# Kernel tuning notes

Measured on AMD Instinct MI355X. Metric: run time of the kernel, lower is better.

Reference implementation:

```python
import jax, jax.numpy as jnp
import numpy as np

IN_FEATURES = 256
EMBED = 512
HEADS = 8
HEAD_DIM = EMBED // HEADS
BLOCKS = 2
FFN = 2048
CLASSES = 1000
NWIRES = 8
BATCH = 8
SEQ = 2048


def _posenc(seq, dim, dtype):
    pos = jnp.arange(seq, dtype=jnp.float32)[:, None]
    div = jnp.exp(jnp.arange(0, dim, 2, dtype=jnp.float32) * (-jnp.log(10000.0) / dim))
    pe = jnp.zeros((seq, dim), dtype=jnp.float32)
    pe = pe.at[:, 0::2].set(jnp.sin(pos * div))
    pe = pe.at[:, 1::2].set(jnp.cos(pos * div))
    return pe.astype(dtype)


def _layer_norm(x, g, b, eps=1e-5):
    mu = jnp.mean(x, axis=-1, keepdims=True)
    var = jnp.var(x, axis=-1, keepdims=True)
    return (x - mu) * jax.lax.rsqrt(var + eps) * g + b


def setup_inputs() -> dict:
    key = jax.random.key(0)
    ks = jax.random.split(key, 20)
    s = 0.02
    inp = {
        'x': jax.random.normal(ks[0], (BATCH, SEQ, IN_FEATURES), dtype=jnp.float32),
        'Wi': jax.random.normal(ks[1], (EMBED, IN_FEATURES), dtype=jnp.float32) * s,
        'bi': jnp.zeros((EMBED,), dtype=jnp.float32),
        'theta_a': jax.random.normal(ks[2], (BLOCKS, NWIRES), dtype=jnp.float32),
        'Wproj': jax.random.normal(ks[3], (BLOCKS, EMBED, NWIRES), dtype=jnp.float32) * s,
        'Wq': jax.random.normal(ks[4], (BLOCKS, EMBED, EMBED), dtype=jnp.float32) * s,
        'Wk': jax.random.normal(ks[5], (BLOCKS, EMBED, EMBED), dtype=jnp.float32) * s,
        'Wv': jax.random.normal(ks[6], (BLOCKS, EMBED, EMBED), dtype=jnp.float32) * s,
        'Wo': jax.random.normal(ks[7], (BLOCKS, EMBED, EMBED), dtype=jnp.float32) * s,
        'g1': jnp.ones((BLOCKS, EMBED), dtype=jnp.float32),
        'b1': jnp.zeros((BLOCKS, EMBED), dtype=jnp.float32),
        'phi': jax.random.normal(ks[8], (BLOCKS, NWIRES), dtype=jnp.float32),
        'W1': jax.random.normal(ks[9], (BLOCKS, FFN, NWIRES), dtype=jnp.float32) * s,
        'W2': jax.random.normal(ks[10], (BLOCKS, EMBED, FFN), dtype=jnp.float32) * s,
        'g2': jnp.ones((BLOCKS, EMBED), dtype=jnp.float32),
        'b2': jnp.zeros((BLOCKS, EMBED), dtype=jnp.float32),
        'Wc': jax.random.normal(ks[11], (CLASSES, EMBED), dtype=jnp.float32) * s,
        'bc': jnp.zeros((CLASSES,), dtype=jnp.float32),
    }
    return inp


def reference(x, Wi, bi, theta_a, Wproj, Wq, Wk, Wv, Wo, g1, b1, phi, W1, W2, g2, b2, Wc, bc):
    b, s, _ = x.shape
    h = jnp.einsum('bsf,ef->bse', x, Wi) + bi          # input_proj
    h = h + _posenc(s, EMBED, h.dtype)[None]           # positional encoding
    scale = 1.0 / np.sqrt(HEAD_DIM)
    for l in range(BLOCKS):
        # --- quantum attention sublayer ---
        # RX encode first NWIRES features + trainable RX per wire -> <Z> = cos(x + theta)
        q_out = jnp.cos(h[..., :NWIRES] + theta_a[l])  # [b,s,nw]
        x_q = jnp.einsum('bsw,ew->bse', q_out, Wproj[l])
        q = jnp.einsum('bse,fe->bsf', x_q, Wq[l]).reshape(b, s, HEADS, HEAD_DIM).transpose(0, 2, 1, 3)
        k = jnp.einsum('bse,fe->bsf', x_q, Wk[l]).reshape(b, s, HEADS, HEAD_DIM).transpose(0, 2, 1, 3)
        v = jnp.einsum('bse,fe->bsf', x_q, Wv[l]).reshape(b, s, HEADS, HEAD_DIM).transpose(0, 2, 1, 3)
        scores = jnp.einsum('bhqd,bhkd->bhqk', q, k) * scale
        attn = jax.nn.softmax(scores, axis=-1)
        out = jnp.einsum('bhqk,bhkd->bhqd', attn, v)
        out = out.transpose(0, 2, 1, 3).reshape(b, s, EMBED)
        attn_out = jnp.einsum('bse,fe->bsf', out, Wo[l])
        h = _layer_norm(h + attn_out, g1[l], b1[l])
        # --- quantum feed-forward sublayer ---
        # RY encode + trainable RY per wire -> <Z> = cos(x + phi)
        qf = jnp.cos(h[..., :NWIRES] + phi[l])         # [b,s,nw]
        f = jnp.einsum('bsw,fw->bsf', qf, W1[l])       # nw -> ffn
        f = jnp.einsum('bsf,ef->bse', jax.nn.relu(f), W2[l])
        h = _layer_norm(h + f, g2[l], b2[l])
    pooled = jnp.mean(h, axis=1)                        # [b, embed]
    logits = jnp.einsum('be,ce->bc', pooled, Wc) + bc
    return logits
```

## Files before the change

kernel.cpp:

```cpp
#include <hip/hip_runtime.h>
#include <hip/hip_bf16.h>
#include <math.h>

#define B_   8
#define S_   2048
#define T_   (B_*S_)
#define FIN  256
#define E_   512
#define H_   8
#define D_   64
#define FFN_ 2048
#define NC_  1000
#define NW_  8

typedef __attribute__((ext_vector_type(8))) short short8;
typedef __attribute__((ext_vector_type(4))) short short4v;
typedef __attribute__((ext_vector_type(4))) float f32x4;
typedef __attribute__((ext_vector_type(2))) unsigned int uint2v;
typedef __attribute__((ext_vector_type(4))) unsigned int uint4v;

__device__ __forceinline__ unsigned short f2bf(float f) {
    __hip_bfloat16 h = __float2bfloat16(f);
    return __builtin_bit_cast(unsigned short, h);
}
__device__ __forceinline__ float bf2f(unsigned short u) {
    return __builtin_bit_cast(float, (unsigned int)u << 16);
}

__device__ __forceinline__ unsigned cvtpk_bf16(float lo, float hi) {
    unsigned r;
    asm("v_cvt_pk_bf16_f32 %0, %1, %2" : "=v"(r) : "v"(lo), "v"(hi));
    return r;
}

#if defined(__has_builtin)
#if __has_builtin(__builtin_amdgcn_permlane32_swap) && __has_builtin(__builtin_amdgcn_permlane16_swap)
#define HAVE_PLSWAP 1
#endif
#endif

__device__ __forceinline__ void lswap32(unsigned &a, unsigned &b) {
#if defined(HAVE_PLSWAP)
    uint2v t = __builtin_amdgcn_permlane32_swap(a, b, false, false);
    a = t[0]; b = t[1];
#else
    unsigned as = (unsigned)__shfl_xor((int)a, 32);
    unsigned bs = (unsigned)__shfl_xor((int)b, 32);
    bool hi = (threadIdx.x & 32) != 0;
    unsigned na = hi ? bs : a;
    unsigned nb = hi ? b  : as;
    a = na; b = nb;
#endif
}
__device__ __forceinline__ void lswap16(unsigned &a, unsigned &b) {
#if defined(HAVE_PLSWAP)
    uint2v t = __builtin_amdgcn_permlane16_swap(a, b, false, false);
    a = t[0]; b = t[1];
#else
    unsigned as = (unsigned)__shfl_xor((int)a, 16);
    unsigned bs = (unsigned)__shfl_xor((int)b, 16);
    bool hi = (threadIdx.x & 16) != 0;
    unsigned na = hi ? bs : a;
    unsigned nb = hi ? b  : as;
    a = na; b = nb;
#endif
}

__device__ __forceinline__ void gld16(void* l, const void* g) {
    __builtin_amdgcn_global_load_lds(
        (const __attribute__((address_space(1))) unsigned int*)g,
        (__attribute__((address_space(3))) unsigned int*)l,
        16, 0, 0);
}

#if defined(__has_builtin)
#if __has_builtin(__builtin_amdgcn_mfma_f32_16x16x16bf16_1k)
#define HAVE_MFMA16 1
#endif
#endif

__device__ __forceinline__ f32x4 mfma16(short4v a, short4v b, f32x4 c) {
#ifdef HAVE_MFMA16
    return __builtin_amdgcn_mfma_f32_16x16x16bf16_1k(a, b, c, 0, 0, 0);
#else
    short8 a8 = {a[0], a[1], a[2], a[3], 0, 0, 0, 0};
    short8 b8 = {b[0], b[1], b[2], b[3], 0, 0, 0, 0};
    return __builtin_amdgcn_mfma_f32_16x16x32_bf16(a8, b8, c, 0, 0, 0);
#endif
}

__global__ __launch_bounds__(256)
void cvt_all(const float* __restrict__ x,  const float* __restrict__ Wi,
             const float* __restrict__ Wo, const float* __restrict__ W2,
             const float* __restrict__ W1,
             unsigned short* xb, unsigned short* Wib,
             unsigned short* Wob, unsigned short* W2b, unsigned short* W1b)
{
    int g = blockIdx.x*256 + threadIdx.x;
    const float* s; unsigned short* d; int o;
    if      (g < 1048576) { s = x;  d = xb;  o = g; }
    else if (g < 1081344) { s = Wi; d = Wib; o = g - 1048576; }
    else if (g < 1212416) { s = Wo; d = Wob; o = g - 1081344; }
    else if (g < 1736704) { s = W2; d = W2b; o = g - 1212416; }
    else                  { s = W1; d = W1b; o = g - 1736704; }
    float4 vv = ((const float4*)s)[o];
    ushort4 u;
    u.x = f2bf(vv.x); u.y = f2bf(vv.y); u.z = f2bf(vv.z); u.w = f2bf(vv.w);
    ((ushort4*)d)[o] = u;
}

__global__ __launch_bounds__(64)
void weff_kernel(const float* __restrict__ Wq, const float* __restrict__ Wk,
                 const float* __restrict__ Wv, const float* __restrict__ Wproj,
                 unsigned short* __restrict__ Weff)
{
    const int f = blockIdx.x, l = blockIdx.y, which = blockIdx.z;
    const int lane = threadIdx.x;
    const float* W = (which == 0 ? Wq : which == 1 ? Wk : Wv)
                     + (size_t)l*E_*E_ + (size_t)f*E_;
    const float* P = Wproj + (size_t)l*E_*NW_;
    const int wv = lane & 7;
    float s = 0.f;
    for (int e = (lane >> 3)*64; e < (lane >> 3)*64 + 64; e++)
        s += W[e] * P[e*NW_ + wv];
    #pragma unroll
    for (int off = 8; off < 64; off <<= 1) s += __shfl_xor(s, off);
    const float scale = (which == 0) ? 0.18033688011112042f : 1.f;
    if (lane < 8)
        Weff[((size_t)(which*2 + l)*E_ + f)*NW_ + lane] = f2bf(s * scale);
}

__global__ __launch_bounds__(64)
void gram_kernel(const unsigned short* __restrict__ Weff, unsigned short* __restrict__ G)
{
    const int hh = blockIdx.x, l = blockIdx.y;
    const int lane = threadIdx.x;
    const int w = lane >> 3, wp = lane & 7;
    const unsigned short* Wq_e = Weff + (size_t)(0*2 + l)*E_*NW_ + (size_t)hh*64*NW_;
    const unsigned short* Wk_e = Weff + (size_t)(1*2 + l)*E_*NW_ + (size_t)hh*64*NW_;
    float s = 0.f;
    for (int d = 0; d < 64; d++)
        s += bf2f(Wq_e[d*NW_ + w]) * bf2f(Wk_e[d*NW_ + wp]);
    G[(size_t)(l*8 + hh)*64 + w*8 + wp] = f2bf(s);
}

__global__ __launch_bounds__(64)
void wov_kernel(const float* __restrict__ Wo, const unsigned short* __restrict__ Weff,
                unsigned short* __restrict__ WoV)
{
    const int f = blockIdx.x, l = blockIdx.y;
    const int lane = threadIdx.x;
    const int hh = lane >> 3, w = lane & 7;
    const float* wrow = Wo + (size_t)l*E_*E_ + (size_t)f*E_ + hh*64;
    const unsigned short* Wv_e = Weff + (size_t)(2*2 + l)*E_*NW_ + (size_t)hh*64*NW_;
    float s = 0.f;
    for (int d = 0; d < 64; d++)
        s += wrow[d] * bf2f(Wv_e[d*NW_ + w]);
    WoV[(size_t)(l*E_ + f)*64 + lane] = f2bf(s);
}

__global__ __launch_bounds__(256)
void qc_small(const unsigned short* __restrict__ h, const float* __restrict__ theta,
              const unsigned short* __restrict__ G,
              unsigned short* __restrict__ c8, unsigned short* __restrict__ c8T,
              unsigned short* __restrict__ gkb)
{
    const int tid = threadIdx.x;
    const int t0 = blockIdx.x * 32;
    __shared__ float cs[32][8];
    __shared__ float Gs[512];
    {
        int tl = tid >> 3, wv2 = tid & 7;
        cs[tl][wv2] = cosf(bf2f(h[(size_t)(t0 + tl)*E_ + wv2]) + theta[wv2]);
        Gs[tid]       = bf2f(G[tid]);
        Gs[tid + 256] = bf2f(G[tid + 256]);
    }
    __syncthreads();
    const int tl = tid >> 3, hh = tid & 7;
    const int bb = (t0 + tl) >> 11, ss = (t0 + tl) & (S_ - 1);
    float c[8];
    #pragma unroll
    for (int i = 0; i < 8; i++) c[i] = cs[tl][i];
    unsigned short u[8] __attribute__((aligned(16)));
    #pragma unroll
    for (int w = 0; w < 8; w++) {
        float s = 0.f;
        #pragma unroll
        for (int wp = 0; wp < 8; wp++) s += Gs[hh*64 + w*8 + wp] * c[wp];
        u[w] = f2bf(s);
    }
    *(float4*)&gkb[((size_t)(bb*H_ + hh)*S_ + ss)*8] = *(float4*)u;
    if (tid < 32) {
        unsigned short v[8] __attribute__((aligned(16)));
        #pragma unroll
        for (int i = 0; i < 8; i++) v[i] = f2bf(cs[tid][i]);
        *(float4*)&c8[(size_t)(t0 + tid)*8] = *(float4*)v;
    } else if (tid < 40) {
        int w = tid - 32;
        unsigned short v[32] __attribute__((aligned(16)));
        #pragma unroll
        for (int s = 0; s < 32; s++) v[s] = f2bf(cs[s][w]);
        unsigned short* dst = c8T + ((size_t)(t0 >> 11)*8 + w)*S_ + (t0 & (S_ - 1));
        #pragma unroll
        for (int cq = 0; cq < 4; cq++) *(float4*)(dst + cq*8) = *(float4*)&v[cq*8];
    }
}

template<int TC_BF16, int MODE>
__global__ __launch_bounds__(256)
void gemm_mfma(const unsigned short* __restrict__ A,
               const unsigned short* __restrict__ Bm,
               void* __restrict__ Cv, int M, int N, int K,
               float scale, const float* __restrict__ bias)
{
    __shared__ char Lraw[32768];
    unsigned short* Al = (unsigned short*)Lraw;
    unsigned short* Bl = (unsigned short*)(Lraw + 16384);
    float* Ot = (float*)Lraw;

    const int tid  = threadIdx.x;
    const int lane = tid & 63;
    const int w    = tid >> 6;
    const int wx   = w & 1, wy = w >> 1;
    int bx, by;
    {
        int nx = gridDim.x;
        int bid = blockIdx.y * nx + blockIdx.x;
        int rpx = gridDim.y >> 3;
        int xcd = bid & 7, idx = bid >> 3;
        by = xcd * rpx + idx / nx;
        bx = idx % nx;
    }
    const int rowBase = by * 128;
    const int colBase = bx * 128;
    const int l15  = lane & 15;
    const int quad = lane >> 4;
    const int srow = lane >> 2;
    const int gch  = (lane & 3) ^ ((srow >> 1) & 3);
    const int swz  = (l15 >> 1) & 3;

    f32x4 acc[4][4] = {};

    #pragma unroll
    for (int it = 0; it < 2; it++) {
        int rb = it*64 + w*16;
        gld16(&Al[rb*32], A  + (size_t)(rowBase + rb + srow)*K + gch*8);
        gld16(&Bl[rb*32], Bm + (size_t)(colBase + rb + srow)*K + gch*8);
    }

    for (int k0 = 0; k0 < K; k0 += 32) {
        const int cur = (k0 >> 5) & 1;
        __syncthreads();
        if (k0 + 32 < K) {
            #pragma unroll
            for (int it = 0; it < 2; it++) {
                int rb = it*64 + w*16;
                gld16(&Al[(1-cur)*4096 + rb*32], A  + (size_t)(rowBase + rb + srow)*K + k0 + 32 + gch*8);
                gld16(&Bl[(1-cur)*4096 + rb*32], Bm + (size_t)(colBase + rb + srow)*K + k0 + 32 + gch*8);
            }
        }
        short8 af[4], bfr[4];
        #pragma unroll
        for (int mi = 0; mi < 4; mi++)
            af[mi] = *(const short8*)&Al[cur*4096 + (wy*64 + mi*16 + l15)*32 + ((quad ^ swz) << 3)];
        #pragma unroll
        for (int ni = 0; ni < 4; ni++)
            bfr[ni] = *(const short8*)&Bl[cur*4096 + (wx*64 + ni*16 + l15)*32 + ((quad ^ swz) << 3)];
        #pragma unroll
        for (int mi = 0; mi < 4; mi++)
            #pragma unroll
            for (int ni = 0; ni < 4; ni++)
                acc[mi][ni] = __builtin_amdgcn_mfma_f32_16x16x32_bf16(
                    af[mi], bfr[ni], acc[mi][ni], 0, 0, 0);
    }

    #pragma unroll
    for (int mi = 0; mi < 4; mi++) {
        __syncthreads();
        #pragma unroll
        for (int ni = 0; ni < 4; ni++) {
            #pragma unroll
            for (int r = 0; r < 4; r++) {
                float v = acc[mi][ni][r] * scale;
                if (MODE == 1) {
                    int row = rowBase + wy*64 + mi*16 + quad*4 + r;
                    int col = colBase + wx*64 + ni*16 + l15;
                    int s = row & (S_ - 1);
                    float freq = __expf(-0.017988946039244957f * (float)(col & ~1));
                    float ang = (float)s * freq;
                    v += bias[col] + ((col & 1) ? cosf(ang) : sinf(ang));
                }
                Ot[(wy*16 + quad*4 + r)*132 + wx*64 + ni*16 + l15] = v;
            }
        }
        __syncthreads();
        {
            int rl = tid >> 3, c0 = (tid & 7) * 16;
            int grow = rowBase + (rl >> 4)*64 + mi*16 + (rl & 15);
            float vv[16];
            #pragma unroll
            for (int j = 0; j < 4; j++)
                *(float4*)&vv[j*4] = *(const float4*)&Ot[rl*132 + c0 + j*4];
            if (TC_BF16) {
                unsigned short u[16] __attribute__((aligned(16)));
                #pragma unroll
                for (int i = 0; i < 16; i++) u[i] = f2bf(vv[i]);
                unsigned short* dst = (unsigned short*)Cv + (size_t)grow*N + colBase + c0;
                *(float4*)dst       = *(float4*)&u[0];
                *(float4*)(dst + 8) = *(float4*)&u[8];
            } else {
                float* dst = (float*)Cv + (size_t)grow*N + colBase + c0;
                #pragma unroll
                for (int j = 0; j < 4; j++)
                    *(float4*)(dst + j*4) = *(const float4*)&vv[j*4];
            }
        }
    }
}

__global__ __launch_bounds__(256)
void wo_ln(const unsigned short* __restrict__ yout,
           const unsigned short* __restrict__ WoV,
           unsigned short* __restrict__ h,
           const float* __restrict__ g, const float* __restrict__ b)
{
    __shared__ float Ot[16*520];
    const int tid  = threadIdx.x;
    const int lane = tid & 63;
    const int w    = tid >> 6;
    const int l15  = lane & 15;
    const int quad = lane >> 4;
    const size_t t0 = (size_t)blockIdx.x * 32;

    short8 af[2][2];
    #pragma unroll
    for (int mi = 0; mi < 2; mi++)
        #pragma unroll
        for (int kb = 0; kb < 2; kb++)
            af[mi][kb] = *(const short8*)&yout[(t0 + mi*16 + l15)*64 + kb*32 + quad*8];

    f32x4 acc[2][8] = {};
    #pragma unroll
    for (int ni = 0; ni < 8; ni++)
        #pragma unroll
        for (int kb = 0; kb < 2; kb++) {
            short8 bf8 = *(const short8*)&WoV[(size_t)(w*128 + ni*16 + l15)*64 + kb*32 + quad*8];
            acc[0][ni] = __builtin_amdgcn_mfma_f32_16x16x32_bf16(af[0][kb], bf8, acc[0][ni], 0, 0, 0);
            acc[1][ni] = __builtin_amdgcn_mfma_f32_16x16x32_bf16(af[1][kb], bf8, acc[1][ni], 0, 0, 0);
        }

    #pragma unroll
    for (int p = 0; p < 2; p++) {
        __syncthreads();
        #pragma unroll
        for (int ni = 0; ni < 8; ni++)
            #pragma unroll
            for (int r = 0; r < 4; r++)
                Ot[(quad*4 + r)*520 + w*128 + ni*16 + l15] = acc[p][ni][r];
        __syncthreads();
        const int tk = tid >> 4, u = tid & 15;
        const size_t trow = t0 + p*16 + tk;
        float x[32];
        float s = 0.f, sq = 0.f;
        #pragma unroll
        for (int j = 0; j < 8; j++) {
            int c = u*4 + j*64;
            ushort4 hv = *(const ushort4*)&h[trow*E_ + c];
            float4 at = *(const float4*)&Ot[tk*520 + c];
            float v0 = bf2f(hv.x) + at.x;
            float v1 = bf2f(hv.y) + at.y;
            float v2 = bf2f(hv.z) + at.z;
            float v3 = bf2f(hv.w) + at.w;
            x[j*4+0] = v0; x[j*4+1] = v1; x[j*4+2] = v2; x[j*4+3] = v3;
            s  += v0 + v1 + v2 + v3;
            sq += v0*v0 + v1*v1 + v2*v2 + v3*v3;
        }
        #pragma unroll
        for (int off = 1; off < 16; off <<= 1) {
            s  += __shfl_xor(s,  off);
            sq += __shfl_xor(sq, off);
        }
        float mu   = s * (1.f/E_);
        float var  = sq * (1.f/E_) - mu*mu;
        float rstd = rsqrtf(var + 1e-5f);
        #pragma unroll
        for (int j = 0; j < 8; j++) {
            int c = u*4 + j*64;
            float4 gv = *(const float4*)&g[c];
            float4 bv = *(const float4*)&b[c];
            ushort4 ov;
            ov.x = f2bf((x[j*4+0] - mu)*rstd*gv.x + bv.x);
            ov.y = f2bf((x[j*4+1] - mu)*rstd*gv.y + bv.y);
            ov.z = f2bf((x[j*4+2] - mu)*rstd*gv.z + bv.z);
            ov.w = f2bf((x[j*4+3] - mu)*rstd*gv.w + bv.w);
            *(ushort4*)&h[trow*E_ + c] = ov;
        }
    }
}

__global__ __launch_bounds__(256)
void gemm_w2f(const unsigned short* __restrict__ h, const float* __restrict__ phi,
              const unsigned short* __restrict__ W1b,
              const unsigned short* __restrict__ W2b,
              unsigned short* __restrict__ tmp)
{
    __shared__ char Lraw[17408];
    unsigned short* Wl = (unsigned short*)Lraw;
    float* Ot = (float*)Lraw;

    const int tid  = threadIdx.x;
    const int lane = tid & 63;
    const int w    = tid >> 6;
    const int tx   = w & 1, ty = w >> 1;
    const int l15  = lane & 15;
    const int quad = lane >> 4;
    const int srow = lane >> 2;
    const int gch  = (lane & 3) ^ ((srow >> 1) & 3);
    const int swz  = (l15 >> 1) & 3;

    const int bid = blockIdx.x;
    const int xcd = bid & 7;
    const int eb  = xcd >> 1;
    const int tb  = (xcd & 1) * 128 + (bid >> 3);
    const int tBase = tb * 64;
    const int eBase = eb * 128;

    short4v cosfr[2];
    #pragma unroll
    for (int nt = 0; nt < 2; nt++) {
        short4v c = {0,0,0,0};
        if (quad < 2) {
            int tok = tBase + ty*32 + nt*16 + l15;
            #pragma unroll
            for (int i = 0; i < 4; i++) {
                int wv = quad*4 + i;
                c[i] = (short)f2bf(cosf(bf2f(h[(size_t)tok*E_ + wv]) + phi[wv]));
            }
        }
        cosfr[nt] = c;
    }

    #pragma unroll
    for (int it = 0; it < 2; it++) {
        int rb = w*32 + it*16;
        gld16(&Wl[rb*32], W2b + (size_t)(eBase + rb + srow)*FFN_ + gch*8);
    }

    const f32x4 fzero = {0.f, 0.f, 0.f, 0.f};
    short4v w1fA[2] = {{0,0,0,0},{0,0,0,0}};

    auto ffn1_pack = [&](short8* pfr_out) {
        unsigned Pm[2][4];
        #pragma unroll
        for (int nt = 0; nt < 2; nt++) {
            #pragma unroll
            for (int jb = 0; jb < 2; jb++) {
                f32x4 c = mfma16(w1fA[jb], cosfr[nt], fzero);
                Pm[nt][jb*2]   = cvtpk_bf16(fmaxf(c[0], 0.f), fmaxf(c[1], 0.f));
                Pm[nt][jb*2+1] = cvtpk_bf16(fmaxf(c[2], 0.f), fmaxf(c[3], 0.f));
            }
            lswap32(Pm[nt][0], Pm[nt][2]); lswap32(Pm[nt][1], Pm[nt][3]);
            lswap16(Pm[nt][0], Pm[nt][2]); lswap16(Pm[nt][1], Pm[nt][3]);
            uint4v u = { Pm[nt][0], Pm[nt][1], Pm[nt][2], Pm[nt][3] };
            pfr_out[nt] = __builtin_bit_cast(short8, u);
        }
    };
    auto load_w1f = [&](int k0) {
        #pragma unroll
        for (int jb = 0; jb < 2; jb++)
            if (quad < 2)
                w1fA[jb] = *(const short4v*)&W1b[(size_t)(k0 + jb*16 + l15)*NW_ + quad*4];
    };

    load_w1f(0);
    short8 pf_cur[2], pf_next[2];
    ffn1_pack(pf_cur);
    load_w1f(32);

    f32x4 acc[4][2] = {};

    for (int k0 = 0; k0 < FFN_; k0 += 32) {
        const int cur = (k0 >> 5) & 1;
        __syncthreads();
        if (k0 + 32 < FFN_) {
            #pragma unroll
            for (int it = 0; it < 2; it++) {
                int rb = w*32 + it*16;
                gld16(&Wl[(1-cur)*4096 + rb*32],
                      W2b + (size_t)(eBase + rb + srow)*FFN_ + k0 + 32 + gch*8);
            }
            ffn1_pack(pf_next);
            if (k0 + 64 < FFN_) load_w1f(k0 + 64);
        }
        #pragma unroll
        for (int et = 0; et < 4; et++) {
            short8 wf = *(const short8*)&Wl[cur*4096 + (tx*64 + et*16 + l15)*32
                                             + ((quad ^ swz) << 3)];
            #pragma unroll
            for (int nt = 0; nt < 2; nt++)
                acc[et][nt] = __builtin_amdgcn_mfma_f32_16x16x32_bf16(
                    wf, pf_cur[nt], acc[et][nt], 0, 0, 0);
        }
        #pragma unroll
        for (int nt = 0; nt < 2; nt++) pf_cur[nt] = pf_next[nt];
    }

    #pragma unroll
    for (int et = 0; et < 4; et++) {
        __syncthreads();
        #pragma unroll
        for (int nt = 0; nt < 2; nt++)
            #pragma unroll
            for (int r = 0; r < 4; r++)
                Ot[(ty*32 + nt*16 + l15)*33 + tx*16 + quad*4 + r] = acc[et][nt][r];
        __syncthreads();
        int token = tid >> 2, q4 = tid & 3;
        unsigned short u[8] __attribute__((aligned(16)));
        #pragma unroll
        for (int i = 0; i < 8; i++) u[i] = f2bf(Ot[token*33 + q4*8 + i]);
        unsigned short* dst = tmp + (size_t)(tBase + token)*E_ + eBase
                              + (q4 >> 1)*64 + et*16 + (q4 & 1)*8;
        *(float4*)dst = *(float4*)&u[0];
    }
}

__global__ __launch_bounds__(256)
void flash_q(const unsigned short* __restrict__ c8,
             const unsigned short* __restrict__ c8T,
             const unsigned short* __restrict__ gkb,
             unsigned short* __restrict__ yout)
{
    const int tid  = threadIdx.x;
    const int lane = tid & 63;
    const int wv   = tid >> 6;
    const int l15  = lane & 15;
    const int quad = lane >> 4;
    const int bid  = blockIdx.x;
    const int xcd  = bid & 7;
    const int rest = bid >> 3;
    const int combo = xcd * 8 + (rest >> 4);
    const int qt = rest & 15;
    const int hh = combo & 7;
    const int bb = combo >> 3;
    const size_t qrow0 = (size_t)bb*S_ + (size_t)qt*128;
    const unsigned short* gkp  = gkb + (size_t)(bb*H_ + hh)*S_*NW_;
    const unsigned short* c8Tp = c8T + (size_t)bb*8*S_;

    short4v cqfr[2] = {{0,0,0,0},{0,0,0,0}};
    if (quad < 2) {
        #pragma unroll
        for (int mi = 0; mi < 2; mi++)
            cqfr[mi] = *(const short4v*)&c8[(qrow0 + wv*32 + mi*16 + l15)*NW_ + quad*4];
    }
    const short8 ones8 = {(short)0x3F80, (short)0x3F80, (short)0x3F80, (short)0x3F80,
                          (short)0x3F80, (short)0x3F80, (short)0x3F80, (short)0x3F80};
    f32x4 y[2] = {};

    for (int kt = 0; kt < S_/64; kt++) {
        f32x4 Sc[2][4] = {};
        #pragma unroll
        for (int nt = 0; nt < 4; nt++) {
            short4v gkf = {0,0,0,0};
            if (quad < 2)
                gkf = *(const short4v*)&gkp[(size_t)(kt*64 + nt*16 + l15)*NW_ + quad*4];
            Sc[0][nt] = mfma16(gkf, cqfr[0], Sc[0][nt]);
            Sc[1][nt] = mfma16(gkf, cqfr[1], Sc[1][nt]);
        }
        unsigned Pm[2][8];
        #pragma unroll
        for (int mi = 0; mi < 2; mi++)
            #pragma unroll
            for (int nt = 0; nt < 4; nt++) {
                float e0 = __builtin_amdgcn_exp2f(Sc[mi][nt][0]);
                float e1 = __builtin_amdgcn_exp2f(Sc[mi][nt][1]);
                float e2 = __builtin_amdgcn_exp2f(Sc[mi][nt][2]);
                float e3 = __builtin_amdgcn_exp2f(Sc[mi][nt][3]);
                Pm[mi][nt*2]   = cvtpk_bf16(e0, e1);
                Pm[mi][nt*2+1] = cvtpk_bf16(e2, e3);
            }
        #pragma unroll
        for (int mi = 0; mi < 2; mi++) {
            lswap32(Pm[mi][0], Pm[mi][2]); lswap32(Pm[mi][1], Pm[mi][3]);
            lswap32(Pm[mi][4], Pm[mi][6]); lswap32(Pm[mi][5], Pm[mi][7]);
            lswap16(Pm[mi][0], Pm[mi][2]); lswap16(Pm[mi][1], Pm[mi][3]);
            lswap16(Pm[mi][4], Pm[mi][6]); lswap16(Pm[mi][5], Pm[mi][7]);
        }
        short8 pf[2][2];
        #pragma unroll
        for (int mi = 0; mi < 2; mi++)
            #pragma unroll
            for (int kb = 0; kb < 2; kb++) {
                uint4v u = { Pm[mi][kb*4], Pm[mi][kb*4+1], Pm[mi][kb*4+2], Pm[mi][kb*4+3] };
                pf[mi][kb] = __builtin_bit_cast(short8, u);
            }
        #pragma unroll
        for (int kb = 0; kb < 2; kb++) {
            short8 a8 = {0,0,0,0,0,0,0,0};
            if (l15 < 8)
                a8 = *(const short8*)&c8Tp[(size_t)l15*S_ + kt*64 + kb*32 + quad*8];
            else if (l15 == 8)
                a8 = ones8;
            y[0] = __builtin_amdgcn_mfma_f32_16x16x32_bf16(a8, pf[0][kb], y[0], 0, 0, 0);
            y[1] = __builtin_amdgcn_mfma_f32_16x16x32_bf16(a8, pf[1][kb], y[1], 0, 0, 0);
        }
    }

    #pragma unroll
    for (int mi = 0; mi < 2; mi++) {
        float rs = __shfl(y[mi][0], 32 + l15);
        float inv = 1.f / rs;
        if (quad < 2) {
            unsigned d0 = cvtpk_bf16(y[mi][0]*inv, y[mi][1]*inv);
            unsigned d1 = cvtpk_bf16(y[mi][2]*inv, y[mi][3]*inv);
            unsigned* dst = (unsigned*)&yout[(qrow0 + wv*32 + mi*16 + l15)*64 + hh*8 + quad*4];
            dst[0] = d0; dst[1] = d1;
        }
    }
}

__global__ __launch_bounds__(256)
void add_ln(unsigned short* __restrict__ h, const unsigned short* __restrict__ delta,
            const float* __restrict__ g, const float* __restrict__ b)
{
    const int lane = threadIdx.x & 63;
    const int t = blockIdx.x*4 + (threadIdx.x >> 6);
    const size_t base = (size_t)t*E_ + lane*8;
    uint4 hv = *(const uint4*)&h[base];
    uint4 dv = *(const uint4*)&delta[base];
    float x[8];
    #pragma unroll
    for (int i = 0; i < 4; i++) {
        unsigned hu = ((const unsigned*)&hv)[i], du = ((const unsigned*)&dv)[i];
        x[2*i]   = bf2f((unsigned short)(hu & 0xffff)) + bf2f((unsigned short)(du & 0xffff));
        x[2*i+1] = bf2f((unsigned short)(hu >> 16))    + bf2f((unsigned short)(du >> 16));
    }
    float s = 0.f, sq = 0.f;
    #pragma unroll
    for (int i = 0; i < 8; i++) { s += x[i]; sq += x[i]*x[i]; }
    #pragma unroll
    for (int off = 1; off < 64; off <<= 1) {
        s  += __shfl_xor(s,  off);
        sq += __shfl_xor(sq, off);
    }
    float mu  = s * (1.f/E_);
    float var = sq * (1.f/E_) - mu*mu;
    float rstd = rsqrtf(var + 1e-5f);
    float4 g0 = *(const float4*)&g[lane*8], g1 = *(const float4*)&g[lane*8 + 4];
    float4 b0 = *(const float4*)&b[lane*8], b1 = *(const float4*)&b[lane*8 + 4];
    float gg[8] = {g0.x,g0.y,g0.z,g0.w,g1.x,g1.y,g1.z,g1.w};
    float bb[8] = {b0.x,b0.y,b0.z,b0.w,b1.x,b1.y,b1.z,b1.w};
    uint4 ov;
    #pragma unroll
    for (int i = 0; i < 4; i++) {
        unsigned lo = f2bf((x[2*i]   - mu)*rstd*gg[2*i]   + bb[2*i]);
        unsigned hi = f2bf((x[2*i+1] - mu)*rstd*gg[2*i+1] + bb[2*i+1]);
        ((unsigned*)&ov)[i] = lo | (hi << 16);
    }
    *(uint4*)&h[base] = ov;
}

__global__ __launch_bounds__(256)
void pool_partial(const unsigned short* __restrict__ h, float* __restrict__ part)
{
    const int chunk = blockIdx.x, bb = blockIdx.y, tid = threadIdx.x;
    for (int e = tid; e < E_; e += 256) {
        const unsigned short* p = h + ((size_t)bb*S_ + (size_t)chunk*128)*E_ + e;
        float s = 0.f;
        for (int r = 0; r < 128; r++) s += bf2f(p[(size_t)r*E_]);
        part[(size_t)(bb*16 + chunk)*E_ + e] = s;
    }
}

__global__ __launch_bounds__(256)
void pool_final(const float* __restrict__ part, float* __restrict__ pooled)
{
    const int bb = blockIdx.x, tid = threadIdx.x;
    for (int e = tid; e < E_; e += 256) {
        float s = 0.f;
        #pragma unroll
        for (int c = 0; c < 16; c++) s += part[(size_t)(bb*16 + c)*E_ + e];
        pooled[bb*E_ + e] = s * (1.f/S_);
    }
}

__global__ __launch_bounds__(64)
void classify(const float* __restrict__ pooled, const float* __restrict__ Wc,
              const float* __restrict__ bc, float* __restrict__ out)
{
    const int c = blockIdx.x, bb = blockIdx.y, lane = threadIdx.x;
    const float* p = pooled + bb*E_;
    const float* wc = Wc + (size_t)c*E_;
    float s = 0.f;
    for (int e = lane; e < E_; e += 64) s += p[e]*wc[e];
    #pragma unroll
    for (int off = 1; off < 64; off <<= 1) s += __shfl_xor(s, off);
    if (lane == 0) out[bb*NC_ + c] = s + bc[c];
}

extern "C" void kernel_launch(void* const* d_in, const int* in_sizes, int n_in,
                              void* d_out, int out_size, void* d_ws, size_t ws_size,
                              hipStream_t stream)
{
    const float* x       = (const float*)d_in[0];
    const float* Wi      = (const float*)d_in[1];
    const float* bi      = (const float*)d_in[2];
    const float* theta_a = (const float*)d_in[3];
    const float* Wproj   = (const float*)d_in[4];
    const float* Wq      = (const float*)d_in[5];
    const float* Wk      = (const float*)d_in[6];
    const float* Wv      = (const float*)d_in[7];
    const float* Wo      = (const float*)d_in[8];
    const float* g1      = (const float*)d_in[9];
    const float* b1      = (const float*)d_in[10];
    const float* phi     = (const float*)d_in[11];
    const float* W1      = (const float*)d_in[12];
    const float* W2      = (const float*)d_in[13];
    const float* g2      = (const float*)d_in[14];
    const float* b2      = (const float*)d_in[15];
    const float* Wc      = (const float*)d_in[16];
    const float* bc      = (const float*)d_in[17];
    float* out = (float*)d_out;

    char* ws = (char*)d_ws;
    const size_t MB = 1024u*1024u;
    unsigned short* h      = (unsigned short*)(ws + 0*MB);
    unsigned short* tmp    = (unsigned short*)(ws + 16*MB);
    unsigned short* c8     = (unsigned short*)(ws + 32*MB);
    unsigned short* c8T    = (unsigned short*)(ws + 33*MB);
    unsigned short* gkb    = (unsigned short*)(ws + 34*MB);
    unsigned short* yout   = (unsigned short*)(ws + 48*MB);
    unsigned short* xb     = (unsigned short*)(ws + 96*MB);
    unsigned short* Wib    = (unsigned short*)(ws + 104*MB);
    unsigned short* Wob    = (unsigned short*)(ws + 105*MB);
    unsigned short* W2b    = (unsigned short*)(ws + 106*MB);
    unsigned short* W1b    = (unsigned short*)(ws + 110*MB);
    unsigned short* Weff   = (unsigned short*)(ws + 111*MB);
    unsigned short* Gbuf   = (unsigned short*)(ws + 111*MB + 64*1024);
    unsigned short* WoV    = (unsigned short*)(ws + 111*MB + 128*1024);
    float*          part   = (float*)(ws + 112*MB);
    float*          pooled = (float*)(ws + 112*MB + 512*1024);

    cvt_all<<<6816, 256, 0, stream>>>(x, Wi, Wo, W2, W1, xb, Wib, Wob, W2b, W1b);
    weff_kernel<<<dim3(E_, 2, 3), 64, 0, stream>>>(Wq, Wk, Wv, Wproj, Weff);
    gram_kernel<<<dim3(H_, 2), 64, 0, stream>>>(Weff, Gbuf);
    wov_kernel<<<dim3(E_, 2), 64, 0, stream>>>(Wo, Weff, WoV);

    gemm_mfma<1,1><<<dim3(E_/128, T_/128), 256, 0, stream>>>(
        xb, Wib, h, T_, E_, FIN, 1.f, bi);

    for (int l = 0; l < 2; l++) {
        qc_small<<<T_/32, 256, 0, stream>>>(h, theta_a + l*NW_, Gbuf + (size_t)l*512,
                                            c8, c8T, gkb);
        flash_q<<<(S_/128)*H_*B_, 256, 0, stream>>>(c8, c8T, gkb, yout);
        wo_ln<<<T_/32, 256, 0, stream>>>(yout, WoV + (size_t)l*E_*64, h,
                                         g1 + l*E_, b1 + l*E_);

        gemm_w2f<<<1024, 256, 0, stream>>>(h, phi + l*NW_,
                                           W1b + (size_t)l*FFN_*NW_,
                                           W2b + (size_t)l*E_*FFN_, tmp);
        add_ln<<<T_/4, 256, 0, stream>>>(h, tmp, g2 + l*E_, b2 + l*E_);
    }

    pool_partial<<<dim3(16, B_), 256, 0, stream>>>(h, part);
    pool_final<<<B_, 256, 0, stream>>>(part, pooled);
    classify<<<dim3(NC_, B_), 64, 0, stream>>>(pooled, Wc, bc, out);
}
```

Before: 560.6 us.

## Fuse FFN W2 GEMM with residual add and LayerNorm per full-row token tile

The W2 GEMM kernel now computes all 512 output columns for a 32-token tile, so the residual add and LayerNorm can run in its epilogue, which lets the separate add_ln kernel and the tmp round trip through global memory be removed. The FFN1 activations are recomputed each k-step instead of being software-pipelined, and the unused Wo bf16 conversion is dropped from cvt_all. In exchange, each block now streams the whole W2 matrix, LDS use grows to about 65KB, and the tiles are smaller (32 tokens), which may lower occupancy and add W2 traffic. The kernel reads h and writes h in place, which is safe only because each block reads its cos inputs and residual from its own rows.

```diff
diff --git a/kernel.cpp b/kernel.cpp
--- a/kernel.cpp
+++ b/kernel.cpp
@@ -91,18 +91,16 @@
 
 __global__ __launch_bounds__(256)
 void cvt_all(const float* __restrict__ x,  const float* __restrict__ Wi,
-             const float* __restrict__ Wo, const float* __restrict__ W2,
-             const float* __restrict__ W1,
+             const float* __restrict__ W2, const float* __restrict__ W1,
              unsigned short* xb, unsigned short* Wib,
-             unsigned short* Wob, unsigned short* W2b, unsigned short* W1b)
+             unsigned short* W2b, unsigned short* W1b)
 {
     int g = blockIdx.x*256 + threadIdx.x;
     const float* s; unsigned short* d; int o;
     if      (g < 1048576) { s = x;  d = xb;  o = g; }
     else if (g < 1081344) { s = Wi; d = Wib; o = g - 1048576; }
-    else if (g < 1212416) { s = Wo; d = Wob; o = g - 1081344; }
-    else if (g < 1736704) { s = W2; d = W2b; o = g - 1212416; }
-    else                  { s = W1; d = W1b; o = g - 1736704; }
+    else if (g < 1605632) { s = W2; d = W2b; o = g - 1081344; }
+    else                  { s = W1; d = W1b; o = g - 1605632; }
     float4 vv = ((const float4*)s)[o];
     ushort4 u;
     u.x = f2bf(vv.x); u.y = f2bf(vv.y); u.z = f2bf(vv.z); u.w = f2bf(vv.w);
@@ -399,19 +397,19 @@
 }
 
 __global__ __launch_bounds__(256)
-void gemm_w2f(const unsigned short* __restrict__ h, const float* __restrict__ phi,
-              const unsigned short* __restrict__ W1b,
-              const unsigned short* __restrict__ W2b,
-              unsigned short* __restrict__ tmp)
-{
-    __shared__ char Lraw[17408];
+void w2f_ln(const unsigned short* __restrict__ hin, const float* __restrict__ phi,
+            const unsigned short* __restrict__ W1b,
+            const unsigned short* __restrict__ W2b,
+            unsigned short* __restrict__ h,
+            const float* __restrict__ g, const float* __restrict__ b)
+{
+    __shared__ char Lraw[66816];
     unsigned short* Wl = (unsigned short*)Lraw;
     float* Ot = (float*)Lraw;
 
     const int tid  = threadIdx.x;
     const int lane = tid & 63;
     const int w    = tid >> 6;
-    const int tx   = w & 1, ty = w >> 1;
     const int l15  = lane & 15;
     const int quad = lane >> 4;
     const int srow = lane >> 2;
@@ -419,108 +417,141 @@
     const int swz  = (l15 >> 1) & 3;
 
     const int bid = blockIdx.x;
-    const int xcd = bid & 7;
-    const int eb  = xcd >> 1;
-    const int tb  = (xcd & 1) * 128 + (bid >> 3);
-    const int tBase = tb * 64;
-    const int eBase = eb * 128;
+    const int tBase = ((bid & 7)*64 + (bid >> 3)) * 32;
 
     short4v cosfr[2];
     #pragma unroll
     for (int nt = 0; nt < 2; nt++) {
         short4v c = {0,0,0,0};
         if (quad < 2) {
-            int tok = tBase + ty*32 + nt*16 + l15;
+            int tok = tBase + nt*16 + l15;
             #pragma unroll
             for (int i = 0; i < 4; i++) {
                 int wv = quad*4 + i;
-                c[i] = (short)f2bf(cosf(bf2f(h[(size_t)tok*E_ + wv]) + phi[wv]));
+                c[i] = (short)f2bf(cosf(bf2f(hin[(size_t)tok*E_ + wv]) + phi[wv]));
             }
         }
         cosfr[nt] = c;
     }
 
     #pragma unroll
-    for (int it = 0; it < 2; it++) {
-        int rb = w*32 + it*16;
-        gld16(&Wl[rb*32], W2b + (size_t)(eBase + rb + srow)*FFN_ + gch*8);
-    }
+    for (int it = 0; it < 8; it++) {
+        int rb = w*128 + it*16;
+        gld16(&Wl[rb*32], W2b + (size_t)(rb + srow)*FFN_ + gch*8);
+    }
+    short4v w1f[2] = {{0,0,0,0},{0,0,0,0}};
+    #pragma unroll
+    for (int jb = 0; jb < 2; jb++)
+        if (quad < 2)
+            w1f[jb] = *(const short4v*)&W1b[(size_t)(jb*16 + l15)*NW_ + quad*4];
 
     const f32x4 fzero = {0.f, 0.f, 0.f, 0.f};
-    short4v w1fA[2] = {{0,0,0,0},{0,0,0,0}};
-
-    auto ffn1_pack = [&](short8* pfr_out) {
-        unsigned Pm[2][4];
-        #pragma unroll
-        for (int nt = 0; nt < 2; nt++) {
-            #pragma unroll
-            for (int jb = 0; jb < 2; jb++) {
-                f32x4 c = mfma16(w1fA[jb], cosfr[nt], fzero);
-                Pm[nt][jb*2]   = cvtpk_bf16(fmaxf(c[0], 0.f), fmaxf(c[1], 0.f));
-                Pm[nt][jb*2+1] = cvtpk_bf16(fmaxf(c[2], 0.f), fmaxf(c[3], 0.f));
-            }
-            lswap32(Pm[nt][0], Pm[nt][2]); lswap32(Pm[nt][1], Pm[nt][3]);
-            lswap16(Pm[nt][0], Pm[nt][2]); lswap16(Pm[nt][1], Pm[nt][3]);
-            uint4v u = { Pm[nt][0], Pm[nt][1], Pm[nt][2], Pm[nt][3] };
-            pfr_out[nt] = __builtin_bit_cast(short8, u);
-        }
-    };
-    auto load_w1f = [&](int k0) {
-        #pragma unroll
-        for (int jb = 0; jb < 2; jb++)
-            if (quad < 2)
-                w1fA[jb] = *(const short4v*)&W1b[(size_t)(k0 + jb*16 + l15)*NW_ + quad*4];
-    };
-
-    load_w1f(0);
-    short8 pf_cur[2], pf_next[2];
-    ffn1_pack(pf_cur);
-    load_w1f(32);
-
-    f32x4 acc[4][2] = {};
+    f32x4 acc[8][2] = {};
 
     for (int k0 = 0; k0 < FFN_; k0 += 32) {
         const int cur = (k0 >> 5) & 1;
         __syncthreads();
         if (k0 + 32 < FFN_) {
             #pragma unroll
-            for (int it = 0; it < 2; it++) {
-                int rb = w*32 + it*16;
-                gld16(&Wl[(1-cur)*4096 + rb*32],
-                      W2b + (size_t)(eBase + rb + srow)*FFN_ + k0 + 32 + gch*8);
-            }
-            ffn1_pack(pf_next);
-            if (k0 + 64 < FFN_) load_w1f(k0 + 64);
-        }
-        #pragma unroll
-        for (int et = 0; et < 4; et++) {
-            short8 wf = *(const short8*)&Wl[cur*4096 + (tx*64 + et*16 + l15)*32
+            for (int it = 0; it < 8; it++) {
+                int rb = w*128 + it*16;
+                gld16(&Wl[(1-cur)*16384 + rb*32],
+                      W2b + (size_t)(rb + srow)*FFN_ + k0 + 32 + gch*8);
+            }
+        }
+        short8 pfr[2];
+        #pragma unroll
+        for (int nt = 0; nt < 2; nt++) {
+            unsigned Pm[4];
+            #pragma unroll
+            for (int jb = 0; jb < 2; jb++) {
+                f32x4 c = mfma16(w1f[jb], cosfr[nt], fzero);
+                Pm[jb*2]   = cvtpk_bf16(fmaxf(c[0], 0.f), fmaxf(c[1], 0.f));
+                Pm[jb*2+1] = cvtpk_bf16(fmaxf(c[2], 0.f), fmaxf(c[3], 0.f));
+            }
+            lswap32(Pm[0], Pm[2]); lswap32(Pm[1], Pm[3]);
+            lswap16(Pm[0], Pm[2]); lswap16(Pm[1], Pm[3]);
+            uint4v u = { Pm[0], Pm[1], Pm[2], Pm[3] };
+            pfr[nt] = __builtin_bit_cast(short8, u);
+        }
+        if (k0 + 32 < FFN_) {
+            #pragma unroll
+            for (int jb = 0; jb < 2; jb++)
+                if (quad < 2)
+                    w1f[jb] = *(const short4v*)&W1b[(size_t)(k0 + 32 + jb*16 + l15)*NW_ + quad*4];
+        }
+        #pragma unroll
+        for (int et = 0; et < 8; et++) {
+            short8 wf = *(const short8*)&Wl[cur*16384 + (w*128 + et*16 + l15)*32
                                              + ((quad ^ swz) << 3)];
             #pragma unroll
             for (int nt = 0; nt < 2; nt++)
                 acc[et][nt] = __builtin_amdgcn_mfma_f32_16x16x32_bf16(
-                    wf, pf_cur[nt], acc[et][nt], 0, 0, 0);
-        }
-        #pragma unroll
-        for (int nt = 0; nt < 2; nt++) pf_cur[nt] = pf_next[nt];
-    }
-
-    #pragma unroll
-    for (int et = 0; et < 4; et++) {
-        __syncthreads();
+                    wf, pfr[nt], acc[et][nt], 0, 0, 0);
+        }
+    }
+
+    __syncthreads();
+    #pragma unroll
+    for (int et = 0; et < 8; et++)
         #pragma unroll
         for (int nt = 0; nt < 2; nt++)
             #pragma unroll
             for (int r = 0; r < 4; r++)
-                Ot[(ty*32 + nt*16 + l15)*33 + tx*16 + quad*4 + r] = acc[et][nt][r];
-        __syncthreads();
-        int token = tid >> 2, q4 = tid & 3;
-        unsigned short u[8] __attribute__((aligned(16)));
-        #pragma unroll
-        for (int i = 0; i < 8; i++) u[i] = f2bf(Ot[token*33 + q4*8 + i]);
-        unsigned short* dst = tmp + (size_t)(tBase + token)*E_ + eBase
-                              + (q4 >> 1)*64 + et*16 + (q4 & 1)*8;
-        *(float4*)dst = *(float4*)&u[0];
+                Ot[(nt*16 + l15)*522 + w*128 + et*16 + quad*4 + r] = acc[et][nt][r];
+    __syncthreads();
+    {
+        const int tk = tid >> 3, u = tid & 7;
+        const size_t trow = (size_t)tBase + tk;
+        float x[64];
+        float s = 0.f, sq = 0.f;
+        #pragma unroll
+        for (int j = 0; j < 8; j++) {
+            int c = u*8 + j*64;
+            short8 hv = *(const short8*)&h[trow*E_ + c];
+            float4 a0 = *(const float4*)&Ot[tk*522 + c];
+            float4 a1 = *(const float4*)&Ot[tk*522 + c + 4];
+            float v[8];
+            v[0] = bf2f((unsigned short)hv[0]) + a0.x;
+            v[1] = bf2f((unsigned short)hv[1]) + a0.y;
+            v[2] = bf2f((unsigned short)hv[2]) + a0.z;
+            v[3] = bf2f((unsigned short)hv[3]) + a0.w;
+            v[4] = bf2f((unsigned short)hv[4]) + a1.x;
+            v[5] = bf2f((unsigned short)hv[5]) + a1.y;
+            v[6] = bf2f((unsigned short)hv[6]) + a1.z;
+            v[7] = bf2f((unsigned short)hv[7]) + a1.w;
+            #pragma unroll
+            for (int i = 0; i < 8; i++) {
+                x[j*8+i] = v[i];
+                s += v[i]; sq += v[i]*v[i];
+            }
+        }
+        #pragma unroll
+        for (int off = 1; off < 8; off <<= 1) {
+            s  += __shfl_xor(s,  off);
+            sq += __shfl_xor(sq, off);
+        }
+        float mu   = s * (1.f/E_);
+        float var  = sq * (1.f/E_) - mu*mu;
+        float rstd = rsqrtf(var + 1e-5f);
+        #pragma unroll
+        for (int j = 0; j < 8; j++) {
+            int c = u*8 + j*64;
+            float4 g0 = *(const float4*)&g[c];
+            float4 g1 = *(const float4*)&g[c + 4];
+            float4 b0 = *(const float4*)&b[c];
+            float4 b1 = *(const float4*)&b[c + 4];
+            unsigned short o[8] __attribute__((aligned(16)));
+            o[0] = f2bf((x[j*8+0] - mu)*rstd*g0.x + b0.x);
+            o[1] = f2bf((x[j*8+1] - mu)*rstd*g0.y + b0.y);
+            o[2] = f2bf((x[j*8+2] - mu)*rstd*g0.z + b0.z);
+            o[3] = f2bf((x[j*8+3] - mu)*rstd*g0.w + b0.w);
+            o[4] = f2bf((x[j*8+4] - mu)*rstd*g1.x + b1.x);
+            o[5] = f2bf((x[j*8+5] - mu)*rstd*g1.y + b1.y);
+            o[6] = f2bf((x[j*8+6] - mu)*rstd*g1.z + b1.z);
+            o[7] = f2bf((x[j*8+7] - mu)*rstd*g1.w + b1.w);
+            *(float4*)&h[trow*E_ + c] = *(float4*)o;
+        }
     }
 }
 
@@ -616,47 +647,6 @@
             dst[0] = d0; dst[1] = d1;
         }
     }
-}
-
-__global__ __launch_bounds__(256)
-void add_ln(unsigned short* __restrict__ h, const unsigned short* __restrict__ delta,
-            const float* __restrict__ g, const float* __restrict__ b)
-{
-    const int lane = threadIdx.x & 63;
-    const int t = blockIdx.x*4 + (threadIdx.x >> 6);
-    const size_t base = (size_t)t*E_ + lane*8;
-    uint4 hv = *(const uint4*)&h[base];
-    uint4 dv = *(const uint4*)&delta[base];
-    float x[8];
-    #pragma unroll
-    for (int i = 0; i < 4; i++) {
-        unsigned hu = ((const unsigned*)&hv)[i], du = ((const unsigned*)&dv)[i];
-        x[2*i]   = bf2f((unsigned short)(hu & 0xffff)) + bf2f((unsigned short)(du & 0xffff));
-        x[2*i+1] = bf2f((unsigned short)(hu >> 16))    + bf2f((unsigned short)(du >> 16));
-    }
-    float s = 0.f, sq = 0.f;
-    #pragma unroll
-    for (int i = 0; i < 8; i++) { s += x[i]; sq += x[i]*x[i]; }
-    #pragma unroll
-    for (int off = 1; off < 64; off <<= 1) {
-        s  += __shfl_xor(s,  off);
-        sq += __shfl_xor(sq, off);
-    }
-    float mu  = s * (1.f/E_);
-    float var = sq * (1.f/E_) - mu*mu;
-    float rstd = rsqrtf(var + 1e-5f);
-    float4 g0 = *(const float4*)&g[lane*8], g1 = *(const float4*)&g[lane*8 + 4];
-    float4 b0 = *(const float4*)&b[lane*8], b1 = *(const float4*)&b[lane*8 + 4];
-    float gg[8] = {g0.x,g0.y,g0.z,g0.w,g1.x,g1.y,g1.z,g1.w};
-    float bb[8] = {b0.x,b0.y,b0.z,b0.w,b1.x,b1.y,b1.z,b1.w};
-    uint4 ov;
-    #pragma unroll
-    for (int i = 0; i < 4; i++) {
-        unsigned lo = f2bf((x[2*i]   - mu)*rstd*gg[2*i]   + bb[2*i]);
-        unsigned hi = f2bf((x[2*i+1] - mu)*rstd*gg[2*i+1] + bb[2*i+1]);
-        ((unsigned*)&ov)[i] = lo | (hi << 16);
-    }
-    *(uint4*)&h[base] = ov;
 }
 
 __global__ __launch_bounds__(256)
@@ -724,14 +714,12 @@
     char* ws = (char*)d_ws;
     const size_t MB = 1024u*1024u;
     unsigned short* h      = (unsigned short*)(ws + 0*MB);
-    unsigned short* tmp    = (unsigned short*)(ws + 16*MB);
     unsigned short* c8     = (unsigned short*)(ws + 32*MB);
     unsigned short* c8T    = (unsigned short*)(ws + 33*MB);
     unsigned short* gkb    = (unsigned short*)(ws + 34*MB);
     unsigned short* yout   = (unsigned short*)(ws + 48*MB);
     unsigned short* xb     = (unsigned short*)(ws + 96*MB);
     unsigned short* Wib    = (unsigned short*)(ws + 104*MB);
-    unsigned short* Wob    = (unsigned short*)(ws + 105*MB);
     unsigned short* W2b    = (unsigned short*)(ws + 106*MB);
     unsigned short* W1b    = (unsigned short*)(ws + 110*MB);
     unsigned short* Weff   = (unsigned short*)(ws + 111*MB);
@@ -740,7 +728,7 @@
     float*          part   = (float*)(ws + 112*MB);
     float*          pooled = (float*)(ws + 112*MB + 512*1024);
 
-    cvt_all<<<6816, 256, 0, stream>>>(x, Wi, Wo, W2, W1, xb, Wib, Wob, W2b, W1b);
+    cvt_all<<<6304, 256, 0, stream>>>(x, Wi, W2, W1, xb, Wib, W2b, W1b);
     weff_kernel<<<dim3(E_, 2, 3), 64, 0, stream>>>(Wq, Wk, Wv, Wproj, Weff);
     gram_kernel<<<dim3(H_, 2), 64, 0, stream>>>(Weff, Gbuf);
     wov_kernel<<<dim3(E_, 2), 64, 0, stream>>>(Wo, Weff, WoV);
@@ -755,10 +743,10 @@
         wo_ln<<<T_/32, 256, 0, stream>>>(yout, WoV + (size_t)l*E_*64, h,
                                          g1 + l*E_, b1 + l*E_);
 
-        gemm_w2f<<<1024, 256, 0, stream>>>(h, phi + l*NW_,
-                                           W1b + (size_t)l*FFN_*NW_,
-                                           W2b + (size_t)l*E_*FFN_, tmp);
-        add_ln<<<T_/4, 256, 0, stream>>>(h, tmp, g2 + l*E_, b2 + l*E_);
+        w2f_ln<<<T_/32, 256, 0, stream>>>(h, phi + l*NW_,
+                                          W1b + (size_t)l*FFN_*NW_,
+                                          W2b + (size_t)l*E_*FFN_, h,
+                                          g2 + l*E_, b2 + l*E_);
     }
 
     pool_partial<<<dim3(16, B_), 256, 0, stream>>>(h, part);
```

Measured after the change: 657.9 us. 1.17x slower.

## Read W2 fragments directly from global memory in FFN GEMM, drop unused Wo conversion

Applied to the files above, without the earlier changes.

The fused FFN kernel no longer stages W2 tiles through double-buffered LDS with per-iteration barriers. Each wave now loads its W2 fragments straight from global memory (relying on L2 reuse) and computes the first FFN projection inline instead of software-pipelining it one step ahead. Separately, the bf16 conversion of Wo, whose result was never used, is removed from the conversion kernel. The risk is that the global loads are uncoalesced and strided by row, and without the prefetch their latency may stall the MFMAs.

```diff
diff --git a/kernel.cpp b/kernel.cpp
--- a/kernel.cpp
+++ b/kernel.cpp
@@ -91,18 +91,16 @@
 
 __global__ __launch_bounds__(256)
 void cvt_all(const float* __restrict__ x,  const float* __restrict__ Wi,
-             const float* __restrict__ Wo, const float* __restrict__ W2,
-             const float* __restrict__ W1,
+             const float* __restrict__ W2, const float* __restrict__ W1,
              unsigned short* xb, unsigned short* Wib,
-             unsigned short* Wob, unsigned short* W2b, unsigned short* W1b)
+             unsigned short* W2b, unsigned short* W1b)
 {
     int g = blockIdx.x*256 + threadIdx.x;
     const float* s; unsigned short* d; int o;
     if      (g < 1048576) { s = x;  d = xb;  o = g; }
     else if (g < 1081344) { s = Wi; d = Wib; o = g - 1048576; }
-    else if (g < 1212416) { s = Wo; d = Wob; o = g - 1081344; }
-    else if (g < 1736704) { s = W2; d = W2b; o = g - 1212416; }
-    else                  { s = W1; d = W1b; o = g - 1736704; }
+    else if (g < 1605632) { s = W2; d = W2b; o = g - 1081344; }
+    else                  { s = W1; d = W1b; o = g - 1605632; }
     float4 vv = ((const float4*)s)[o];
     ushort4 u;
     u.x = f2bf(vv.x); u.y = f2bf(vv.y); u.z = f2bf(vv.z); u.w = f2bf(vv.w);
@@ -404,9 +402,7 @@
               const unsigned short* __restrict__ W2b,
               unsigned short* __restrict__ tmp)
 {
-    __shared__ char Lraw[17408];
-    unsigned short* Wl = (unsigned short*)Lraw;
-    float* Ot = (float*)Lraw;
+    __shared__ float Ot[64*33];
 
     const int tid  = threadIdx.x;
     const int lane = tid & 63;
@@ -414,9 +410,6 @@
     const int tx   = w & 1, ty = w >> 1;
     const int l15  = lane & 15;
     const int quad = lane >> 4;
-    const int srow = lane >> 2;
-    const int gch  = (lane & 3) ^ ((srow >> 1) & 3);
-    const int swz  = (l15 >> 1) & 3;
 
     const int bid = blockIdx.x;
     const int xcd = bid & 7;
@@ -440,69 +433,41 @@
         cosfr[nt] = c;
     }
 
-    #pragma unroll
-    for (int it = 0; it < 2; it++) {
-        int rb = w*32 + it*16;
-        gld16(&Wl[rb*32], W2b + (size_t)(eBase + rb + srow)*FFN_ + gch*8);
-    }
-
     const f32x4 fzero = {0.f, 0.f, 0.f, 0.f};
-    short4v w1fA[2] = {{0,0,0,0},{0,0,0,0}};
-
-    auto ffn1_pack = [&](short8* pfr_out) {
-        unsigned Pm[2][4];
-        #pragma unroll
-        for (int nt = 0; nt < 2; nt++) {
-            #pragma unroll
-            for (int jb = 0; jb < 2; jb++) {
-                f32x4 c = mfma16(w1fA[jb], cosfr[nt], fzero);
-                Pm[nt][jb*2]   = cvtpk_bf16(fmaxf(c[0], 0.f), fmaxf(c[1], 0.f));
-                Pm[nt][jb*2+1] = cvtpk_bf16(fmaxf(c[2], 0.f), fmaxf(c[3], 0.f));
-            }
-            lswap32(Pm[nt][0], Pm[nt][2]); lswap32(Pm[nt][1], Pm[nt][3]);
-            lswap16(Pm[nt][0], Pm[nt][2]); lswap16(Pm[nt][1], Pm[nt][3]);
-            uint4v u = { Pm[nt][0], Pm[nt][1], Pm[nt][2], Pm[nt][3] };
-            pfr_out[nt] = __builtin_bit_cast(short8, u);
-        }
-    };
-    auto load_w1f = [&](int k0) {
+    f32x4 acc[4][2] = {};
+
+    const unsigned short* wbase = W2b + (size_t)(eBase + tx*64 + l15)*FFN_ + quad*8;
+
+    #pragma unroll 2
+    for (int k0 = 0; k0 < FFN_; k0 += 32) {
+        short4v w1f[2] = {{0,0,0,0},{0,0,0,0}};
         #pragma unroll
         for (int jb = 0; jb < 2; jb++)
             if (quad < 2)
-                w1fA[jb] = *(const short4v*)&W1b[(size_t)(k0 + jb*16 + l15)*NW_ + quad*4];
-    };
-
-    load_w1f(0);
-    short8 pf_cur[2], pf_next[2];
-    ffn1_pack(pf_cur);
-    load_w1f(32);
-
-    f32x4 acc[4][2] = {};
-
-    for (int k0 = 0; k0 < FFN_; k0 += 32) {
-        const int cur = (k0 >> 5) & 1;
-        __syncthreads();
-        if (k0 + 32 < FFN_) {
-            #pragma unroll
-            for (int it = 0; it < 2; it++) {
-                int rb = w*32 + it*16;
-                gld16(&Wl[(1-cur)*4096 + rb*32],
-                      W2b + (size_t)(eBase + rb + srow)*FFN_ + k0 + 32 + gch*8);
+                w1f[jb] = *(const short4v*)&W1b[(size_t)(k0 + jb*16 + l15)*NW_ + quad*4];
+        short8 pfr[2];
+        #pragma unroll
+        for (int nt = 0; nt < 2; nt++) {
+            unsigned Pm[4];
+            #pragma unroll
+            for (int jb = 0; jb < 2; jb++) {
+                f32x4 c = mfma16(w1f[jb], cosfr[nt], fzero);
+                Pm[jb*2]   = cvtpk_bf16(fmaxf(c[0], 0.f), fmaxf(c[1], 0.f));
+                Pm[jb*2+1] = cvtpk_bf16(fmaxf(c[2], 0.f), fmaxf(c[3], 0.f));
             }
-            ffn1_pack(pf_next);
-            if (k0 + 64 < FFN_) load_w1f(k0 + 64);
+            lswap32(Pm[0], Pm[2]); lswap32(Pm[1], Pm[3]);
+            lswap16(Pm[0], Pm[2]); lswap16(Pm[1], Pm[3]);
+            uint4v u = { Pm[0], Pm[1], Pm[2], Pm[3] };
+            pfr[nt] = __builtin_bit_cast(short8, u);
         }
         #pragma unroll
         for (int et = 0; et < 4; et++) {
-            short8 wf = *(const short8*)&Wl[cur*4096 + (tx*64 + et*16 + l15)*32
-                                             + ((quad ^ swz) << 3)];
+            short8 wf = *(const short8*)(wbase + (size_t)et*16*FFN_ + k0);
             #pragma unroll
             for (int nt = 0; nt < 2; nt++)
                 acc[et][nt] = __builtin_amdgcn_mfma_f32_16x16x32_bf16(
-                    wf, pf_cur[nt], acc[et][nt], 0, 0, 0);
-        }
-        #pragma unroll
-        for (int nt = 0; nt < 2; nt++) pf_cur[nt] = pf_next[nt];
+                    wf, pfr[nt], acc[et][nt], 0, 0, 0);
+        }
     }
 
     #pragma unroll
@@ -731,7 +696,6 @@
     unsigned short* yout   = (unsigned short*)(ws + 48*MB);
     unsigned short* xb     = (unsigned short*)(ws + 96*MB);
     unsigned short* Wib    = (unsigned short*)(ws + 104*MB);
-    unsigned short* Wob    = (unsigned short*)(ws + 105*MB);
     unsigned short* W2b    = (unsigned short*)(ws + 106*MB);
     unsigned short* W1b    = (unsigned short*)(ws + 110*MB);
     unsigned short* Weff   = (unsigned short*)(ws + 111*MB);
@@ -740,7 +704,7 @@
     float*          part   = (float*)(ws + 112*MB);
     float*          pooled = (float*)(ws + 112*MB + 512*1024);
 
-    cvt_all<<<6816, 256, 0, stream>>>(x, Wi, Wo, W2, W1, xb, Wib, Wob, W2b, W1b);
+    cvt_all<<<6304, 256, 0, stream>>>(x, Wi, W2, W1, xb, Wib, W2b, W1b);
     weff_kernel<<<dim3(E_, 2, 3), 64, 0, stream>>>(Wq, Wk, Wv, Wproj, Weff);
     gram_kernel<<<dim3(H_, 2), 64, 0, stream>>>(Weff, Gbuf);
     wov_kernel<<<dim3(E_, 2), 64, 0, stream>>>(Wo, Weff, WoV);
```

Result: slower. 701.5 us (+25.1%).
